# Kernel optimization log

Measured on AMD Instinct MI355X. Metric: run time of the kernel, lower is better.

## Reference

```python
import jax, jax.numpy as jnp
import numpy as np

K = 1023   # kernel_size == embedding_dim
H = 16     # out_channels (filters per sample)
E = 256    # num_embeddings
T = 8      # num_tokens
CC = 0.25  # commitment cost
EPS = np.float32(np.finfo(np.float32).eps)
DN = ('NCH', 'OIH', 'NCH')


def setup_inputs() -> dict:
    key = jax.random.key(0)
    ks = jax.random.split(key, 10)
    B, C, L = 8, 1, 8184
    D_ff = 2 * E
    X = jax.random.normal(ks[0], (B, C, L), jnp.float32)
    embedding = jax.random.uniform(ks[1], (E, K), jnp.float32, -1.0 / E, 1.0 / E)
    ffn_w1 = jax.random.normal(ks[2], (E, D_ff), jnp.float32) * 0.02
    ffn_b1 = jnp.zeros((D_ff,), jnp.float32)
    ffn_w2 = jax.random.normal(ks[3], (D_ff, E), jnp.float32) * 0.02
    ffn_b2 = jnp.zeros((E,), jnp.float32)
    ln_g = jnp.ones((E,), jnp.float32)
    ln_b = jnp.zeros((E,), jnp.float32)
    cls_w = jax.random.normal(ks[4], (E, 10), jnp.float32) * 0.02
    cls_b = jnp.zeros((10,), jnp.float32)
    return dict(X=X, embedding=embedding, ffn_w1=ffn_w1, ffn_b1=ffn_b1,
                ffn_w2=ffn_w2, ffn_b2=ffn_b2, ln_g=ln_g, ln_b=ln_b,
                cls_w=cls_w, cls_b=cls_b)


def _autocov(f):
    # f: [..., K]. FFT-based autocovariance of hann-windowed, max-normalized frame.
    n = f.shape[-1]
    fmax = jnp.max(jnp.abs(f), axis=-1, keepdims=True)
    fmax = jnp.where(fmax == 0, EPS, fmax)
    win = 0.5 * (1.0 - jnp.cos(2.0 * jnp.pi * jnp.arange(n, dtype=jnp.float32) / n))
    xw = f * win / fmax
    spec = jnp.abs(jnp.fft.rfft(xw, n=n) ** 2)   # |rfft(x)^2| == |rfft(x)|^2
    return jnp.fft.ifftshift(jnp.fft.irfft(spec, n=n), axes=-1)


def reference(X, embedding, ffn_w1, ffn_b1, ffn_w2, ffn_b2, ln_g, ln_b, cls_w, cls_b):
    B, C, L = X.shape
    # ---- encoder: extract frames at fixed linspace positions, autocovariance ----
    Lp = ((L + K - 1) // K) * K          # PadForConv(zero) length (no-op here)
    end = Lp - K - 1 - K
    positions = jnp.linspace(0.0, float(end), H).astype(jnp.int32)
    idx = positions[:, None] + jnp.arange(K)          # (H, K)
    frames = X[:, :, idx]                             # (B, C, H, K) gather
    Z = _autocov(jnp.transpose(frames, (0, 2, 1, 3)))  # (B, H, C, K)
    # ---- VQ: pairwise distances + argmin + codebook lookup ----
    flat = Z.reshape(-1, K)                           # (B*H*C, K)
    d = (jnp.sum(flat ** 2, axis=1, keepdims=True)
         + jnp.sum(embedding ** 2, axis=1)
         - 2.0 * flat @ embedding.T)                  # (B*H*C, E)
    codes = jnp.argmin(d, axis=1)
    enc = jax.nn.one_hot(codes, E, dtype=flat.dtype)
    quant = (enc @ embedding).reshape(Z.shape)
    sg = jax.lax.stop_gradient
    e_loss = jnp.mean((sg(quant) - Z) ** 2)
    q_loss = jnp.mean((quant - sg(Z)) ** 2)
    vq_loss = q_loss + CC * e_loss
    quant_st = Z + sg(quant - Z)                      # straight-through
    avg = jnp.mean(enc, axis=0)
    perplexity = jnp.exp(-jnp.sum(avg * jnp.log(avg + EPS)))
    # ---- decoder: every sample's filter bank convolved with the whole batch ----
    fmerged = quant_st.reshape(B * H, C, K)           # merge per-sample banks
    out = jax.lax.conv_general_dilated(X, fmerged, (1,), 'SAME',
                                       dimension_numbers=DN)  # (B, B*H, L)
    out = out.reshape(B, B, H, L)                     # (batch b, filter-sample i, k, L)
    sq = (out - X[:, None, :, :]) ** 2                # C==1 broadcast
    # sum_i mean_k mse_{b,l} == mean over (b,k,l) then sum over i
    recon_loss = jnp.sum(jnp.mean(sq, axis=(0, 2, 3)))
    # ---- project: conv with codebook as filters ----
    pfilt = jnp.broadcast_to(embedding[:, None, :], (E, C, K))
    proj = jax.lax.conv_general_dilated(X, pfilt, (1,), 'VALID',
                                        dimension_numbers=DN)  # (B, E, Lo)
    Lo = proj.shape[-1]
    pad = ((Lo + T - 1) // T) * T - Lo                # PadForConv(mean)
    m = jnp.mean(proj, axis=-1, keepdims=True)
    proj = jnp.concatenate([proj, jnp.broadcast_to(m, (B, E, pad))], axis=-1)
    # ---- classify ----
    x = proj.reshape(B, E, T, -1).transpose(0, 2, 3, 1)  # (B, T, t, E)
    x = jnp.max(x, axis=2)                               # (B, T, E)
    mu = jnp.mean(x, axis=-1, keepdims=True)
    var = jnp.var(x, axis=-1, keepdims=True)
    xn = (x - mu) / jnp.sqrt(var + 1e-5) * ln_g + ln_b
    hdd = jax.nn.relu(xn @ ffn_w1 + ffn_b1) @ ffn_w2 + ffn_b2
    feat = jnp.mean(hdd, axis=1)                         # (B, E)
    logits = feat @ cls_w + cls_b
    return (logits, vq_loss, recon_loss, perplexity)
```

## Files before the change

kernel.cpp:

```cpp
#include <hip/hip_runtime.h>

#define KK 1023
#define LL 8184
#define LO 7162
#define XPS 10240
#define EPSF 1.1920928955078125e-07f
#define NEG_INF (-3.4028234663852886e+38f)

typedef short bf16x8 __attribute__((ext_vector_type(8)));
typedef float f32x4 __attribute__((ext_vector_type(4)));

__device__ __constant__ int c_pos[16] = {0,409,818,1227,1636,2045,2454,2863,
                                         3273,3682,4091,4500,4909,5318,5727,6137};

__device__ __forceinline__ unsigned short f2bf(float f) {
    unsigned u = __float_as_uint(f);
    unsigned r = (u + 0x7FFFu + ((u >> 16) & 1u)) >> 16;
    return (unsigned short)r;
}
__device__ __forceinline__ int fenc(float f) {
    int u = __float_as_int(f);
    return u >= 0 ? u : (~u) ^ 0x80000000;
}
__device__ __forceinline__ float fdec(int k) {
    int u = k >= 0 ? k : ~(k ^ 0x80000000);
    return __int_as_float(u);
}
__device__ __forceinline__ void gl2lds16(const void* g, void* l) {
    __builtin_amdgcn_global_load_lds(
        (const __attribute__((address_space(1))) void*)g,
        (__attribute__((address_space(3))) void*)l, 16, 0, 0);
}

__global__ __launch_bounds__(256) void k_pa(const float* __restrict__ X,
                                            const float* __restrict__ emb,
                                            unsigned short* __restrict__ Xpad,
                                            unsigned short* __restrict__ Xodd,
                                            unsigned short* __restrict__ Ebf,
                                            float* __restrict__ Etf,
                                            float* __restrict__ enorm,
                                            int* __restrict__ hist,
                                            int* __restrict__ cmax,
                                            float* __restrict__ Z) {
    __shared__ __align__(16) float xw[2046];
    __shared__ float red[256];
    const int q = blockIdx.x;
    const int tid = threadIdx.x;
    if (q < 256) {
        const int fi = q >> 1, half = q & 1;
        const int b = fi >> 4, h = fi & 15;
        const float* xp = X + b * LL + c_pos[h];
        float lmax = 0.f;
        for (int j = tid; j < KK; j += 256) {
            float v = xp[j];
            xw[j] = v;
            lmax = fmaxf(lmax, fabsf(v));
        }
        red[tid] = lmax;
        __syncthreads();
        for (int off = 128; off; off >>= 1) {
            if (tid < off) red[tid] = fmaxf(red[tid], red[tid + off]);
            __syncthreads();
        }
        float fmx = red[0];
        if (fmx == 0.f) fmx = EPSF;
        __syncthreads();
        for (int j = tid; j < KK; j += 256) {
            float v = xw[j];
            float win = 0.5f * (1.0f - cosf(6.28318530717958647692f * (float)j / 1023.0f));
            float w = v * win / fmx;
            xw[j] = w;
            xw[j + KK] = w;
        }
        __syncthreads();

        const int m2 = half * 512 + 2 * tid;
        const int mh = m2 >> 1;
        const float2* X2 = (const float2*)xw;
        float a0 = 0.f, a1 = 0.f;
        float2 F = X2[mh];
#pragma unroll 2
        for (int jh = 0; jh < 510; jh += 2) {
            float2 xj0 = X2[jh];
            float2 xj1 = X2[jh + 1];
            float2 G0 = X2[mh + jh + 1];
            float2 G1 = X2[mh + jh + 2];
            a0 = fmaf(xj0.x, F.x, a0);
            a0 = fmaf(xj0.y, F.y, a0);
            a1 = fmaf(xj0.x, F.y, a1);
            a1 = fmaf(xj0.y, G0.x, a1);
            a0 = fmaf(xj1.x, G0.x, a0);
            a0 = fmaf(xj1.y, G0.y, a0);
            a1 = fmaf(xj1.x, G0.y, a1);
            a1 = fmaf(xj1.y, G1.x, a1);
            F = G1;
        }
        {
            float2 xj = X2[510];
            float2 G = X2[mh + 511];
            a0 = fmaf(xj.x, F.x, a0);
            a0 = fmaf(xj.y, F.y, a0);
            a1 = fmaf(xj.x, F.y, a1);
            a1 = fmaf(xj.y, G.x, a1);
            F = G;
        }
        float xt = xw[1022];
        a0 = fmaf(xt, F.x, a0);
        a1 = fmaf(xt, F.y, a1);
        float* zrow = Z + fi * KK;
        int i0 = m2 + 512; if (i0 >= KK) i0 -= KK;
        zrow[i0] = a0;
        if (m2 + 1 < KK) {
            int i1 = m2 + 513; if (i1 >= KK) i1 -= KK;
            zrow[i1] = a1;
        }
    } else if (q < 288) {
        const int qq = q - 256;
        const int b = qq >> 2, seg = qq & 3;
        for (int i = seg * 2560 + tid; i < (seg + 1) * 2560; i += 256) {
            unsigned short v = 0, vo = 0;
            if (i >= 512 && i < 512 + LL) v = f2bf(X[b * LL + (i - 512)]);
            const int i1 = i + 1;
            if (i1 >= 512 && i1 < 512 + LL) vo = f2bf(X[b * LL + (i1 - 512)]);
            Xpad[b * XPS + i] = v;
            Xodd[b * XPS + i] = vo;
        }
    } else if (q < 544) {
        const int e = q - 288;
        const float* er = emb + e * KK;
        float nrm = 0.f;
        for (int k = tid; k < 1024; k += 256) {
            float v = (k < KK) ? er[k] : 0.f;
            Ebf[e * 1024 + k] = (k < KK) ? f2bf(v) : (unsigned short)0;
            Etf[(k >> 2) * 1024 + e * 4 + (k & 3)] = v;
            nrm = fmaf(v, v, nrm);
        }
        red[tid] = nrm;
        __syncthreads();
        for (int off = 128; off; off >>= 1) {
            if (tid < off) red[tid] += red[tid + off];
            __syncthreads();
        }
        if (tid == 0) enorm[e] = red[0];
    } else {
        const int i = (q - 544) * 256 + tid;
        cmax[i] = INT_MIN;
        if (q == 544) hist[tid] = 0;
    }
}

__global__ __launch_bounds__(256) void k_vq(const float* __restrict__ Z,
                                            const float4* __restrict__ Et4,
                                            const float* __restrict__ enorm,
                                            const float* __restrict__ emb,
                                            int* __restrict__ codes,
                                            int* __restrict__ hist,
                                            float* __restrict__ vq_part) {
    __shared__ float zl[KK];
    __shared__ __align__(16) float zm2[1024];
    __shared__ float rv[256];
    __shared__ int   ri[256];
    const int fi = blockIdx.x, tid = threadIdx.x;
    const float* zrow = Z + fi * KK;
    for (int t = tid; t < 1024; t += 256) {
        float z = (t < KK) ? zrow[t] : 0.f;
        if (t < KK) zl[t] = z;
        zm2[t] = -2.f * z;
    }
    __syncthreads();

    float d = enorm[tid];
    const float4* zp = (const float4*)zm2;
    const float4* ep = Et4 + tid;
#pragma unroll 8
    for (int t4 = 0; t4 < 256; ++t4) {
        float4 ev = ep[t4 * 256];
        float4 zv = zp[t4];
        d = fmaf(zv.x, ev.x, d);
        d = fmaf(zv.y, ev.y, d);
        d = fmaf(zv.z, ev.z, d);
        d = fmaf(zv.w, ev.w, d);
    }
    rv[tid] = d; ri[tid] = tid;
    __syncthreads();
    for (int off = 128; off; off >>= 1) {
        if (tid < off) {
            float v2 = rv[tid + off]; int i2 = ri[tid + off];
            if (v2 < rv[tid] || (v2 == rv[tid] && i2 < ri[tid])) { rv[tid] = v2; ri[tid] = i2; }
        }
        __syncthreads();
    }
    const int code = ri[0];
    if (tid == 0) { codes[fi] = code; atomicAdd(&hist[code], 1); }

    const float* qr = emb + code * KK;
    float s = 0.f;
    for (int t = tid; t < KK; t += 256) { float dd = qr[t] - zl[t]; s += dd * dd; }
    __syncthreads();
    rv[tid] = s;
    __syncthreads();
    for (int off = 128; off; off >>= 1) {
        if (tid < off) rv[tid] += rv[tid + off];
        __syncthreads();
    }
    if (tid == 0) vq_part[fi] = rv[0];
}

__global__ __launch_bounds__(256, 4) void k_gemm(const unsigned short* __restrict__ Xpad,
                                                 const unsigned short* __restrict__ Xodd,
                                                 const unsigned short* __restrict__ Ebf,
                                                 const int* __restrict__ codes,
                                                 const float* __restrict__ X,
                                                 float* __restrict__ psum_part,
                                                 float* __restrict__ recon_part,
                                                 int* __restrict__ cmax) {
    __shared__ __align__(16) unsigned short lds_b[8 * 1280];
    __shared__ __align__(16) unsigned short lds_a[2 * 2048];
    __shared__ float red_s[64][4];
    const int tid  = threadIdx.x;
    const int lane = tid & 63;
    const int c = lane & 15, g = lane >> 4;
    const int wg = tid >> 6;

    const int bi = blockIdx.x;
    const bool isproj = bi < 896;
    int b, l0, row0;
    if (isproj) { b = bi / 112; int r = bi % 112; row0 = (r / 28) * 64; l0 = (r % 28) * 256; }
    else        { int q = bi - 896; b = q >> 6; int r = q & 63; row0 = (r >> 5) * 64; l0 = (r & 31) * 256; }
    const int xw0 = (isproj ? 512 : 0) + l0;

    {
        const unsigned short* base_e = Xpad + b * XPS + xw0;
        const unsigned short* base_o = Xodd + b * XPS + xw0;
        for (int k = tid; k < 1280; k += 256) {
            const int wdw = k / 160;
            const int p = k - wdw * 160;
            const unsigned short* src = (wdw & 1) ? (base_o + wdw - 1 + p * 8)
                                                  : (base_e + wdw + p * 8);
            gl2lds16(src, lds_b + k * 8);
        }
    }
    const int r_lds = tid >> 2, q4 = tid & 3;
    const int grow = isproj ? (row0 + r_lds) : codes[row0 + r_lds];
    const unsigned short* e_src = Ebf + grow * 1024 + q4 * 8;
    gl2lds16(e_src, lds_a + tid * 8);
    __syncthreads();

    f32x4 acc[4][4];
#pragma unroll
    for (int i = 0; i < 4; ++i)
#pragma unroll
        for (int j = 0; j < 4; ++j) acc[i][j] = (f32x4){0.f, 0.f, 0.f, 0.f};

    const char* lax = (const char*)lds_a;
    const char* lbx = (const char*)lds_b;
    const int boff0 = (wg & 1) * 10240 + ((wg >> 1) << 4) + 32 * c + 16 * g;
    const int aoff0 = c * 64 + g * 16;

    for (int s = 0; s < 32; ++s) {
        const int cur = s & 1;
        if (s + 1 < 32)
            gl2lds16(e_src + (s + 1) * 32, lds_a + ((s + 1) & 1) * 2048 + tid * 8);
        const char* ab = lax + cur * 4096 + aoff0;
        bf16x8 af[4];
#pragma unroll
        for (int et = 0; et < 4; ++et) af[et] = *(const bf16x8*)(ab + et * 1024);
#pragma unroll
        for (int ntl = 0; ntl < 4; ++ntl) {
            bf16x8 bfrag = *(const bf16x8*)(lbx + boff0 + ntl * 2560 + 64 * s);
#pragma unroll
            for (int et = 0; et < 4; ++et)
                acc[et][ntl] = __builtin_amdgcn_mfma_f32_16x16x32_bf16(af[et], bfrag, acc[et][ntl], 0, 0, 0);
        }
        __syncthreads();
    }

    const int lseg  = l0 >> 8;
    const int lbase = l0 + wg * 4;
    if (isproj) {
        const int ch0 = lbase / 896;
#pragma unroll
        for (int et = 0; et < 4; ++et) {
#pragma unroll
            for (int r = 0; r < 4; ++r) {
                float ssum = 0.f, m0 = NEG_INF, m1 = NEG_INF;
#pragma unroll
                for (int ntl = 0; ntl < 4; ++ntl) {
                    float v = acc[et][ntl][r];
                    int l = lbase + ntl + 16 * c;
                    bool ok = l < LO;
                    ssum += ok ? v : 0.f;
                    int ch = l / 896;
                    if (ok && ch == ch0) m0 = fmaxf(m0, v);
                    if (ok && ch != ch0) m1 = fmaxf(m1, v);
                }
                ssum += __shfl_xor(ssum, 1); ssum += __shfl_xor(ssum, 2);
                ssum += __shfl_xor(ssum, 4); ssum += __shfl_xor(ssum, 8);
                m0 = fmaxf(m0, __shfl_xor(m0, 1)); m0 = fmaxf(m0, __shfl_xor(m0, 2));
                m0 = fmaxf(m0, __shfl_xor(m0, 4)); m0 = fmaxf(m0, __shfl_xor(m0, 8));
                m1 = fmaxf(m1, __shfl_xor(m1, 1)); m1 = fmaxf(m1, __shfl_xor(m1, 2));
                m1 = fmaxf(m1, __shfl_xor(m1, 4)); m1 = fmaxf(m1, __shfl_xor(m1, 8));
                if (c == 0) {
                    int eidx = et * 16 + g * 4 + r;
                    red_s[eidx][wg] = ssum;
                    int e = row0 + eidx;
                    int cb = (b * 256 + e) * 8;
                    if (m0 > NEG_INF && ch0 < 8)     atomicMax(&cmax[cb + ch0], fenc(m0));
                    if (m1 > NEG_INF && ch0 + 1 < 8) atomicMax(&cmax[cb + ch0 + 1], fenc(m1));
                }
            }
        }
    } else {
        float xv[4];
#pragma unroll
        for (int ntl = 0; ntl < 4; ++ntl) {
            int lr = lbase + ntl + 16 * c - 1;
            xv[ntl] = (lr >= 0 && lr < LL) ? X[b * LL + lr] : 0.f;
        }
#pragma unroll
        for (int et = 0; et < 4; ++et) {
#pragma unroll
            for (int r = 0; r < 4; ++r) {
                float ssum = 0.f;
#pragma unroll
                for (int ntl = 0; ntl < 4; ++ntl) {
                    int lr = lbase + ntl + 16 * c - 1;
                    bool ok = (lr >= 0) && (lr < LL);
                    float dd = ok ? (acc[et][ntl][r] - xv[ntl]) : 0.f;
                    ssum += dd * dd;
                }
                ssum += __shfl_xor(ssum, 1); ssum += __shfl_xor(ssum, 2);
                ssum += __shfl_xor(ssum, 4); ssum += __shfl_xor(ssum, 8);
                if (c == 0) red_s[et * 16 + g * 4 + r][wg] = ssum;
            }
        }
    }
    __syncthreads();
    if (tid < 64) {
        float tot = red_s[tid][0] + red_s[tid][1] + red_s[tid][2] + red_s[tid][3];
        if (isproj) {
            int e = row0 + tid;
            psum_part[lseg * 2048 + b * 256 + e] = tot;
        } else {
            int f = row0 + tid;
            recon_part[(b * 128 + f) * 32 + lseg] = tot;
        }
    }
}

__global__ __launch_bounds__(256) void k_ln(const float* __restrict__ psum_part,
                                            const int* __restrict__ cmax,
                                            const float* __restrict__ ln_g,
                                            const float* __restrict__ ln_b,
                                            float* __restrict__ xn) {
    __shared__ float red[256];
    __shared__ float red2[256];
    const int bt = blockIdx.x;
    const int t = bt & 7;
    const int b = bt >> 3;
    const int e = threadIdx.x;
    const float* ps = psum_part + b * 256 + e;
    float sm = 0.f;
#pragma unroll
    for (int s = 0; s < 28; ++s) sm += ps[s * 2048];
    float m = sm * (1.0f / 7162.0f);
    const int cb = (b * 256 + e) << 3;
    float v = (t < 7) ? fdec(cmax[cb + t]) : fmaxf(fdec(cmax[cb + 7]), m);
    red[e] = v; red2[e] = v * v;
    __syncthreads();
    for (int off = 128; off; off >>= 1) {
        if (e < off) { red[e] += red[e + off]; red2[e] += red2[e + off]; }
        __syncthreads();
    }
    float mu  = red[0] * (1.0f / 256.0f);
    float var = red2[0] * (1.0f / 256.0f) - mu * mu;
    float r = 1.0f / sqrtf(var + 1e-5f);
    xn[bt * 256 + e] = (v - mu) * r * ln_g[e] + ln_b[e];
}

__global__ __launch_bounds__(256) void k_ffn1(const float* __restrict__ xn,
                                              const float* __restrict__ w1,
                                              const float* __restrict__ b1,
                                              float* __restrict__ hbuf) {
    __shared__ float xr[256];
    __shared__ float rv[256];
    const int q = blockIdx.x;
    const int bt = q & 63, jc = q >> 6;
    const int tid = threadIdx.x;
    xr[tid] = xn[bt * 256 + tid];
    __syncthreads();
    const int jj = tid & 63, ks = tid >> 6;
    const int j = jc * 64 + jj;
    const float* wp = w1 + (ks * 64) * 512 + j;
    float a = 0.f;
#pragma unroll
    for (int ee = 0; ee < 64; ++ee) a = fmaf(xr[ks * 64 + ee], wp[ee * 512], a);
    rv[tid] = a;
    __syncthreads();
    if (tid < 64) {
        float s = rv[tid] + rv[tid + 64] + rv[tid + 128] + rv[tid + 192];
        hbuf[bt * 512 + jc * 64 + tid] = fmaxf(s + b1[jc * 64 + tid], 0.f);
    }
}

__global__ __launch_bounds__(256) void k_ffn2(const float* __restrict__ hbuf,
                                              const float* __restrict__ w2,
                                              const float* __restrict__ b2,
                                              float* __restrict__ hdd) {
    __shared__ float hr[512];
    __shared__ float rv[256];
    const int q = blockIdx.x;
    const int bt = q & 63, jc = q >> 6;
    const int tid = threadIdx.x;
    hr[tid] = hbuf[bt * 512 + tid];
    hr[tid + 256] = hbuf[bt * 512 + 256 + tid];
    __syncthreads();
    const int jj = tid & 63, ks = tid >> 6;
    const int e = jc * 64 + jj;
    const float* wp = w2 + (ks * 128) * 256 + e;
    float a = 0.f;
#pragma unroll
    for (int j = 0; j < 128; ++j) a = fmaf(hr[ks * 128 + j], wp[j * 256], a);
    rv[tid] = a;
    __syncthreads();
    if (tid < 64) {
        float s = rv[tid] + rv[tid + 64] + rv[tid + 128] + rv[tid + 192];
        hdd[bt * 256 + jc * 64 + tid] = s + b2[jc * 64 + tid];
    }
}

__global__ __launch_bounds__(256) void k_final(const float* __restrict__ hdd,
                                               const float* __restrict__ cls_w,
                                               const float* __restrict__ cls_b,
                                               const float* __restrict__ recon_part,
                                               const float* __restrict__ vq_part,
                                               const int* __restrict__ hist,
                                               float* __restrict__ out) {
    __shared__ float red[256];
    const int tid = threadIdx.x;
    if (blockIdx.x == 0) {
        __shared__ float feat[8][256];
#pragma unroll
        for (int b2 = 0; b2 < 8; ++b2) {
            float fb = 0.f;
#pragma unroll
            for (int t2 = 0; t2 < 8; ++t2) fb += hdd[(b2 * 8 + t2) * 256 + tid];
            feat[b2][tid] = fb * 0.125f;
        }
        __syncthreads();
        if (tid < 80) {
            const int b = tid / 10, k = tid % 10;
            float a = cls_b[k];
            for (int e = 0; e < 256; ++e) a = fmaf(feat[b][e], cls_w[e * 10 + k], a);
            out[tid] = a;
        }
    } else {
        float s = 0.f;
        for (int i = tid; i < 32768; i += 256) s += recon_part[i];
        red[tid] = s;
        __syncthreads();
        for (int off = 128; off; off >>= 1) { if (tid < off) red[tid] += red[tid + off]; __syncthreads(); }
        if (tid == 0) out[81] = red[0] / 1047552.0f;
        __syncthreads();
        red[tid] = (tid < 128) ? vq_part[tid] : 0.f;
        __syncthreads();
        for (int off = 128; off; off >>= 1) { if (tid < off) red[tid] += red[tid + off]; __syncthreads(); }
        if (tid == 0) out[80] = 1.25f * red[0] / 130944.0f;
        __syncthreads();
        float avg = (float)hist[tid] * (1.0f / 128.0f);
        red[tid] = avg * logf(avg + EPSF);
        __syncthreads();
        for (int off = 128; off; off >>= 1) { if (tid < off) red[tid] += red[tid + off]; __syncthreads(); }
        if (tid == 0) out[82] = expf(-red[0]);
    }
}

extern "C" void kernel_launch(void* const* d_in, const int* in_sizes, int n_in,
                              void* d_out, int out_size, void* d_ws, size_t ws_size,
                              hipStream_t stream) {
    const float* X     = (const float*)d_in[0];
    const float* emb   = (const float*)d_in[1];
    const float* w1    = (const float*)d_in[2];
    const float* b1    = (const float*)d_in[3];
    const float* w2    = (const float*)d_in[4];
    const float* b2    = (const float*)d_in[5];
    const float* ln_g  = (const float*)d_in[6];
    const float* ln_b  = (const float*)d_in[7];
    const float* cls_w = (const float*)d_in[8];
    const float* cls_b = (const float*)d_in[9];
    float* out = (float*)d_out;

    float* Z            = (float*)d_ws;
    float* vq_part      = Z + 130944;
    float* xnbuf        = vq_part + 128;
    float* hdd          = xnbuf + 16384;
    float* psum_part    = hdd + 16384;
    float* recon_part   = psum_part + 65536;
    int*   cmaxb        = (int*)(recon_part + 32768);
    int*   codes        = cmaxb + 16384;
    int*   hist         = codes + 128;
    unsigned short* Xpad = (unsigned short*)(hist + 256);
    unsigned short* Xodd = Xpad + 8 * XPS;
    unsigned short* Ebf  = Xodd + 8 * XPS;
    float* Etf           = (float*)(Ebf + 256 * 1024);
    float* enorm         = Etf + 256 * 1024;
    float* hbuf          = enorm + 256;

    k_pa     <<<dim3(608), dim3(256), 0, stream>>>(X, emb, Xpad, Xodd, Ebf, Etf, enorm, hist, cmaxb, Z);
    k_vq     <<<dim3(128), dim3(256), 0, stream>>>(Z, (const float4*)Etf, enorm, emb, codes, hist, vq_part);
    k_gemm   <<<dim3(1408), dim3(256), 0, stream>>>(Xpad, Xodd, Ebf, codes, X, psum_part, recon_part, cmaxb);
    k_ln     <<<dim3(64),  dim3(256), 0, stream>>>(psum_part, cmaxb, ln_g, ln_b, xnbuf);
    k_ffn1   <<<dim3(512), dim3(256), 0, stream>>>(xnbuf, w1, b1, hbuf);
    k_ffn2   <<<dim3(256), dim3(256), 0, stream>>>(hbuf, w2, b2, hdd);
    k_final  <<<dim3(2),   dim3(256), 0, stream>>>(hdd, cls_w, cls_b, recon_part, vq_part, hist, out);
}
```

Measured before the change: 137.1 us.

## Fuse layernorm into FFN1 and register-block autocov over four lags

Merges the layernorm kernel and the first FFN matmul into one kernel so that each (b,t) block normalizes in LDS and then computes all 512 hidden outputs directly. This removes one launch and the xn round trip through global memory, but it cuts FFN1 parallelism from 512 blocks to 64 blocks with a 256-long serial loop. It also changes the autocovariance inner loop so each thread computes four lags using float4 LDS reads and a sliding register window, halving the active threads to reduce LDS traffic per FMA.

```diff
diff --git a/kernel.cpp b/kernel.cpp
--- a/kernel.cpp
+++ b/kernel.cpp
@@ -42,7 +42,7 @@
                                             int* __restrict__ hist,
                                             int* __restrict__ cmax,
                                             float* __restrict__ Z) {
-    __shared__ __align__(16) float xw[2046];
+    __shared__ __align__(16) float xw[2048];
     __shared__ float red[256];
     const int q = blockIdx.x;
     const int tid = threadIdx.x;
@@ -74,45 +74,64 @@
         }
         __syncthreads();
 
-        const int m2 = half * 512 + 2 * tid;
-        const int mh = m2 >> 1;
-        const float2* X2 = (const float2*)xw;
-        float a0 = 0.f, a1 = 0.f;
-        float2 F = X2[mh];
-#pragma unroll 2
-        for (int jh = 0; jh < 510; jh += 2) {
-            float2 xj0 = X2[jh];
-            float2 xj1 = X2[jh + 1];
-            float2 G0 = X2[mh + jh + 1];
-            float2 G1 = X2[mh + jh + 2];
-            a0 = fmaf(xj0.x, F.x, a0);
-            a0 = fmaf(xj0.y, F.y, a0);
-            a1 = fmaf(xj0.x, F.y, a1);
-            a1 = fmaf(xj0.y, G0.x, a1);
-            a0 = fmaf(xj1.x, G0.x, a0);
-            a0 = fmaf(xj1.y, G0.y, a0);
-            a1 = fmaf(xj1.x, G0.y, a1);
-            a1 = fmaf(xj1.y, G1.x, a1);
-            F = G1;
-        }
-        {
-            float2 xj = X2[510];
-            float2 G = X2[mh + 511];
-            a0 = fmaf(xj.x, F.x, a0);
-            a0 = fmaf(xj.y, F.y, a0);
-            a1 = fmaf(xj.x, F.y, a1);
-            a1 = fmaf(xj.y, G.x, a1);
-            F = G;
-        }
-        float xt = xw[1022];
-        a0 = fmaf(xt, F.x, a0);
-        a1 = fmaf(xt, F.y, a1);
-        float* zrow = Z + fi * KK;
-        int i0 = m2 + 512; if (i0 >= KK) i0 -= KK;
-        zrow[i0] = a0;
-        if (m2 + 1 < KK) {
-            int i1 = m2 + 513; if (i1 >= KK) i1 -= KK;
-            zrow[i1] = a1;
+        if (tid < 128) {
+            const int m = half * 512 + 4 * tid;
+            const int mh = m >> 1;
+            const int mq4 = mh >> 1;
+            const float2* X2 = (const float2*)xw;
+            const float4* X4 = (const float4*)xw;
+            float a0 = 0.f, a1 = 0.f, a2 = 0.f, a3 = 0.f;
+            float2 W0 = X2[mh], W1 = X2[mh + 1], W2 = X2[mh + 2], W3 = X2[mh + 3];
+            for (int jh = 0; jh < 510; jh += 2) {
+                float4 nw = X4[mq4 + (jh >> 1) + 2];
+                float4 xj = X4[jh >> 1];
+                a0 = fmaf(xj.x, W0.x, a0);
+                a0 = fmaf(xj.y, W0.y, a0);
+                a0 = fmaf(xj.z, W1.x, a0);
+                a0 = fmaf(xj.w, W1.y, a0);
+                a1 = fmaf(xj.x, W0.y, a1);
+                a1 = fmaf(xj.y, W1.x, a1);
+                a1 = fmaf(xj.z, W1.y, a1);
+                a1 = fmaf(xj.w, W2.x, a1);
+                a2 = fmaf(xj.x, W1.x, a2);
+                a2 = fmaf(xj.y, W1.y, a2);
+                a2 = fmaf(xj.z, W2.x, a2);
+                a2 = fmaf(xj.w, W2.y, a2);
+                a3 = fmaf(xj.x, W1.y, a3);
+                a3 = fmaf(xj.y, W2.x, a3);
+                a3 = fmaf(xj.z, W2.y, a3);
+                a3 = fmaf(xj.w, W3.x, a3);
+                W0 = W2; W1 = W3;
+                W2 = make_float2(nw.x, nw.y);
+                W3 = make_float2(nw.z, nw.w);
+            }
+            {
+                float2 xj = X2[510];
+                a0 = fmaf(xj.x, W0.x, a0);
+                a0 = fmaf(xj.y, W0.y, a0);
+                a1 = fmaf(xj.x, W0.y, a1);
+                a1 = fmaf(xj.y, W1.x, a1);
+                a2 = fmaf(xj.x, W1.x, a2);
+                a2 = fmaf(xj.y, W1.y, a2);
+                a3 = fmaf(xj.x, W1.y, a3);
+                a3 = fmaf(xj.y, W2.x, a3);
+            }
+            float xt = xw[1022];
+            a0 = fmaf(xt, W1.x, a0);
+            a1 = fmaf(xt, W1.y, a1);
+            a2 = fmaf(xt, W2.x, a2);
+            a3 = fmaf(xt, W2.y, a3);
+
+            float* zrow = Z + fi * KK;
+            float av[4] = {a0, a1, a2, a3};
+#pragma unroll
+            for (int qq = 0; qq < 4; ++qq) {
+                int mmq = m + qq;
+                if (mmq < KK) {
+                    int i0 = mmq + 512; if (i0 >= KK) i0 -= KK;
+                    zrow[i0] = av[qq];
+                }
+            }
         }
     } else if (q < 288) {
         const int qq = q - 256;
@@ -348,13 +367,16 @@
     }
 }
 
-__global__ __launch_bounds__(256) void k_ln(const float* __restrict__ psum_part,
-                                            const int* __restrict__ cmax,
-                                            const float* __restrict__ ln_g,
-                                            const float* __restrict__ ln_b,
-                                            float* __restrict__ xn) {
+__global__ __launch_bounds__(256) void k_lnffn1(const float* __restrict__ psum_part,
+                                                const int* __restrict__ cmax,
+                                                const float* __restrict__ ln_g,
+                                                const float* __restrict__ ln_b,
+                                                const float* __restrict__ w1,
+                                                const float* __restrict__ b1,
+                                                float* __restrict__ hbuf) {
     __shared__ float red[256];
     __shared__ float red2[256];
+    __shared__ float xr[256];
     const int bt = blockIdx.x;
     const int t = bt & 7;
     const int b = bt >> 3;
@@ -375,32 +397,18 @@
     float mu  = red[0] * (1.0f / 256.0f);
     float var = red2[0] * (1.0f / 256.0f) - mu * mu;
     float r = 1.0f / sqrtf(var + 1e-5f);
-    xn[bt * 256 + e] = (v - mu) * r * ln_g[e] + ln_b[e];
-}
-
-__global__ __launch_bounds__(256) void k_ffn1(const float* __restrict__ xn,
-                                              const float* __restrict__ w1,
-                                              const float* __restrict__ b1,
-                                              float* __restrict__ hbuf) {
-    __shared__ float xr[256];
-    __shared__ float rv[256];
-    const int q = blockIdx.x;
-    const int bt = q & 63, jc = q >> 6;
-    const int tid = threadIdx.x;
-    xr[tid] = xn[bt * 256 + tid];
-    __syncthreads();
-    const int jj = tid & 63, ks = tid >> 6;
-    const int j = jc * 64 + jj;
-    const float* wp = w1 + (ks * 64) * 512 + j;
-    float a = 0.f;
-#pragma unroll
-    for (int ee = 0; ee < 64; ++ee) a = fmaf(xr[ks * 64 + ee], wp[ee * 512], a);
-    rv[tid] = a;
-    __syncthreads();
-    if (tid < 64) {
-        float s = rv[tid] + rv[tid + 64] + rv[tid + 128] + rv[tid + 192];
-        hbuf[bt * 512 + jc * 64 + tid] = fmaxf(s + b1[jc * 64 + tid], 0.f);
-    }
+    xr[e] = (v - mu) * r * ln_g[e] + ln_b[e];
+    __syncthreads();
+
+    float a0 = 0.f, a1 = 0.f;
+#pragma unroll 4
+    for (int ee = 0; ee < 256; ++ee) {
+        float xv = xr[ee];
+        a0 = fmaf(xv, w1[ee * 512 + e], a0);
+        a1 = fmaf(xv, w1[ee * 512 + 256 + e], a1);
+    }
+    hbuf[bt * 512 + e]       = fmaxf(a0 + b1[e], 0.f);
+    hbuf[bt * 512 + 256 + e] = fmaxf(a1 + b1[256 + e], 0.f);
 }
 
 __global__ __launch_bounds__(256) void k_ffn2(const float* __restrict__ hbuf,
@@ -509,8 +517,7 @@
     k_pa     <<<dim3(608), dim3(256), 0, stream>>>(X, emb, Xpad, Xodd, Ebf, Etf, enorm, hist, cmaxb, Z);
     k_vq     <<<dim3(128), dim3(256), 0, stream>>>(Z, (const float4*)Etf, enorm, emb, codes, hist, vq_part);
     k_gemm   <<<dim3(1408), dim3(256), 0, stream>>>(Xpad, Xodd, Ebf, codes, X, psum_part, recon_part, cmaxb);
-    k_ln     <<<dim3(64),  dim3(256), 0, stream>>>(psum_part, cmaxb, ln_g, ln_b, xnbuf);
-    k_ffn1   <<<dim3(512), dim3(256), 0, stream>>>(xnbuf, w1, b1, hbuf);
+    k_lnffn1 <<<dim3(64),  dim3(256), 0, stream>>>(psum_part, cmaxb, ln_g, ln_b, w1, b1, hbuf);
     k_ffn2   <<<dim3(256), dim3(256), 0, stream>>>(hbuf, w2, b2, hdd);
     k_final  <<<dim3(2),   dim3(256), 0, stream>>>(hdd, cls_w, cls_b, recon_part, vq_part, hist, out);
 }
```

Result: no change. 139.9 us (+2.0%).
